# Kernel tuning notes

Hardware: AMD Instinct MI355X
Metric: run time of the kernel (lower is better)

## Reference

```python
import jax, jax.numpy as jnp
import numpy as np

N_HEADS = 4
N_NODES = 10000
EMB = 128
N_BATCH = 4096
N_NEAREST = 8
N_SENTINELS = 8


def setup_inputs() -> dict:
    key = jax.random.key(0)
    k1, k2, k3, k4 = jax.random.split(key, 4)
    embeds = jax.random.normal(k1, (N_HEADS, N_NODES, EMB), jnp.float32)
    field = jax.random.uniform(k3, (N_HEADS, N_NODES, EMB), dtype=jnp.float32)
    uncertainty = jnp.ones((1, 1, 1), jnp.float32) * 5.0
    adj = (jax.random.uniform(k4, (N_NODES, N_NODES)) < 0.001).astype(jnp.float32)
    batch_edges = jax.random.randint(k2, (2, N_BATCH), 0, N_NODES)
    return {"embeds": embeds, "field": field, "uncertainty": uncertainty,
            "adj": adj, "batch_edges": batch_edges}


def _knn_samples(embeds, nodes, k):
    # embeds: (h, n, d); nodes: (b,) -> indices of k nearest neighbors, excluding self.
    # Squared L2 distance is monotone in L2 norm, so top-k order matches the
    # original's .norm(dim=3).topk(..., largest=False).
    x = embeds[:, nodes]                                  # (h, b, d)
    x2 = jnp.sum(x * x, axis=-1)[:, :, None]              # (h, b, 1)
    y2 = jnp.sum(embeds * embeds, axis=-1)[:, None, :]    # (h, 1, n)
    d2 = x2 + y2 - 2.0 * jnp.einsum('hbd,hnd->hbn', x, embeds)  # (h, b, n)
    _, idx = jax.lax.top_k(-d2, k + 1)                    # nearest first
    return jax.lax.stop_gradient(idx[:, :, 1:])           # drop self -> (h, b, k)


def reference(embeds, field, uncertainty, adj, batch_edges):
    src, dst = batch_edges[0], batch_edges[1]
    h_idx = jnp.arange(N_HEADS)[:, None, None]

    def build(nodes, nodes_logits, adj_gather):
        samples = _knn_samples(embeds, nodes, N_NEAREST)                 # (h,b,k)
        diff = embeds[:, nodes][:, :, None, :] - embeds[h_idx, samples]  # (h,b,k,d)
        label = uncertainty * (adj_gather(samples) * 2.0 - 1.0)          # (h,b,k)
        g = field[:, nodes_logits]                                        # (h,b,d)
        logits = jnp.einsum('hbkd,hbd->hbk', diff, g) + label
        return logits, diff

    src_logits, src_diff = build(src, dst, lambda s: adj[s, dst[None, :, None]])
    tgt_logits, tgt_diff = build(dst, src, lambda s: adj[src[None, :, None], s])

    logits = jnp.concatenate([src_logits, tgt_logits], axis=2)           # (h,b,2k)
    dist = jnp.linalg.norm(jnp.concatenate([src_diff, tgt_diff], axis=2), axis=3)

    h, b = logits.shape[0], logits.shape[1]
    logits = jnp.concatenate(
        [logits, jnp.zeros((h, b, N_SENTINELS), logits.dtype)], axis=2)
    dist = jnp.concatenate(
        [dist, jnp.ones((h, b, N_SENTINELS), dist.dtype)], axis=2)

    # softmin: softmax(1 - dist)-weighted sum of logits, then mean over heads
    softmin = jnp.sum(logits * jax.nn.softmax(1.0 - dist, axis=2), axis=2)  # (h,b)
    return jax.nn.sigmoid(softmin.mean(axis=0)).reshape(-1)                 # (b,)
```

## Files before the change

kernel.cpp:

```cpp
#include <hip/hip_runtime.h>
#include <math.h>
#include <stdint.h>

#define N_HEADS 4
#define N_NODES 10000
#define NPAD 10112
#define NPG (NPAD / 32)
#define EMB 128
#define N_BATCH 4096
#define NQ (2 * N_BATCH)
#define K 8
#define TQ 64
#define TN 128
#define NTILES (NPAD / TN)
#define PH 2
#define CAP 41
#define WIN 0.5f

typedef __attribute__((ext_vector_type(8))) __bf16 bf16x8;
typedef __attribute__((ext_vector_type(8))) unsigned short ushortx8;
typedef __attribute__((ext_vector_type(16))) float floatx16;

__device__ __forceinline__ unsigned short f2bf(float x) {
  unsigned u = __float_as_uint(x);
  u += 0x7fff + ((u >> 16) & 1);
  return (unsigned short)(u >> 16);
}
__device__ __forceinline__ uint32_t bfup(float f) {
  uint32_t u = __float_as_uint(f);
  return (f >= 0.f) ? ((u + 0xFFFFu) >> 16) : (u >> 16);
}

__device__ __forceinline__ void insert8(float* bs, int* bi, float s, int node) {
  if (s < bs[K - 1]) {
    #pragma unroll
    for (int k2 = K - 1; k2 >= 0; --k2) {
      if (!(s < bs[k2])) break;
      if (k2 < K - 1) { bs[k2 + 1] = bs[k2]; bi[k2 + 1] = bi[k2]; }
      bs[k2] = s; bi[k2] = node;
    }
  }
}

__device__ __forceinline__ size_t pchunk(int g, int c, int lm) {
  return (size_t)g * 4096 + (size_t)(c >> 1) * 512 + (size_t)(c & 1) * 256 + lm * 8;
}

__global__ __launch_bounds__(256) void prep_kernel(
    const float* __restrict__ E, unsigned short* __restrict__ EhiP,
    float* __restrict__ y2g) {
  __shared__ float s_p[8][33];
  const int h = blockIdx.y, g = blockIdx.x;
  const int lm = threadIdx.x & 31, c8 = threadIdx.x >> 5;
  const int n = g * 32 + lm;
  float x[16];
  #pragma unroll
  for (int j = 0; j < 16; ++j) x[j] = 0.f;
  if (n < N_NODES) {
    const float* src = E + (size_t)(h * N_NODES + n) * EMB + c8 * 16;
    #pragma unroll
    for (int j = 0; j < 4; ++j) {
      float4 v = *(const float4*)(src + j * 4);
      x[j * 4 + 0] = v.x; x[j * 4 + 1] = v.y; x[j * 4 + 2] = v.z; x[j * 4 + 3] = v.w;
    }
  }
  float part = 0.f;
  ushortx8 hi[2];
  #pragma unroll
  for (int j = 0; j < 16; ++j) {
    part += x[j] * x[j];
    hi[j >> 3][j & 7] = f2bf(x[j]);
  }
  size_t base = (size_t)h * NPG * 4096;
  #pragma unroll
  for (int lh = 0; lh < 2; ++lh)
    *(ushortx8*)&EhiP[base + pchunk(g, c8 * 2 + lh, lm)] = hi[lh];
  s_p[c8][lm] = part;
  __syncthreads();
  if (threadIdx.x < 32) {
    int nn = g * 32 + threadIdx.x;
    float s = 0.f;
    #pragma unroll
    for (int j = 0; j < 8; ++j) s += s_p[j][threadIdx.x];
    y2g[h * NPAD + nn] = (nn < N_NODES) ? s : 1e30f;
  }
}

__global__ __launch_bounds__(256)
__attribute__((amdgpu_waves_per_eu(2, 2)))
void knn_kernel(
    const unsigned short* __restrict__ EhiP, const float* __restrict__ y2g,
    const float* __restrict__ Ef, const int* __restrict__ be,
    int* __restrict__ samples) {
  __shared__ __align__(16) float s_x[TQ * TN];
  __shared__ float s_t8S[TQ * 9];
  __shared__ int   s_t8I[TQ * 9];
  __shared__ float s_lsS[TQ * CAP];
  __shared__ int   s_lsI[TQ * CAP];
  __shared__ float s_thr[TQ];
  __shared__ int   s_cnt[TQ];

  const int id = blockIdx.x;
  const int h = (id & 7) >> 1;
  const int qt = ((id >> 3) << 1) | (id & 1);
  const int tid = threadIdx.x;
  const int lane = tid & 63;
  const int w1 = tid >> 6;
  const int lm = lane & 31, lh = lane >> 5;
  const unsigned short* EhiH = EhiP + (size_t)h * NPG * 4096;
  const float* y2H = y2g + h * NPAD;
  const float* EH = Ef + (size_t)h * N_NODES * EMB;

  bf16x8 a0[8], a1[8];
  {
    int q0 = be[qt * TQ + lm];
    int q1 = be[qt * TQ + 32 + lm];
    int g0 = q0 >> 5, l0 = q0 & 31;
    int g1 = q1 >> 5, l1 = q1 & 31;
    #pragma unroll
    for (int ks = 0; ks < 8; ++ks) {
      a0[ks] = *(const bf16x8*)&EhiH[pchunk(g0, ks * 2 + lh, l0)];
      a1[ks] = *(const bf16x8*)&EhiH[pchunk(g1, ks * 2 + lh, l1)];
    }
  }

  const int qsel = tid >> 2;
  const int csel = tid & 3;
  const int myq = be[qt * TQ + qsel];
  float bs[K]; int bi[K];
  #pragma unroll
  for (int k2 = 0; k2 < K; ++k2) { bs[k2] = 1e30f; bi[k2] = 0x7fffffff; }
  if (tid < TQ) s_cnt[tid] = 0;

  const int bnode = 32 * w1 + lm;
  const unsigned short* bhp = EhiH + (size_t)w1 * 4096 + lane * 8;

  #pragma unroll 1
  for (int t = 0; t < PH; ++t) {
    const size_t goff = (size_t)t * 16384;
    float ny = y2H[t * TN + bnode];
    floatx16 acc0 = {0.f, 0.f, 0.f, 0.f, 0.f, 0.f, 0.f, 0.f,
                     0.f, 0.f, 0.f, 0.f, 0.f, 0.f, 0.f, 0.f};
    floatx16 acc1 = acc0;
    #pragma unroll
    for (int ks = 0; ks < 8; ++ks) {
      bf16x8 vbh = *(const bf16x8*)(bhp + goff + ks * 512);
      acc0 = __builtin_amdgcn_mfma_f32_32x32x16_bf16(a0[ks], vbh, acc0, 0, 0, 0);
      acc1 = __builtin_amdgcn_mfma_f32_32x32x16_bf16(a1[ks], vbh, acc1, 0, 0, 0);
    }
    #pragma unroll
    for (int r = 0; r < 16; ++r) {
      int row = (r & 3) + 8 * (r >> 2) + 4 * lh;
      s_x[row * TN + bnode] = fmaf(-2.f, acc0[r], ny);
      s_x[(row + 32) * TN + bnode] = fmaf(-2.f, acc1[r], ny);
    }
    __syncthreads();
    int nbp = t * TN;
    #pragma unroll
    for (int s = 0; s < 32; ++s) {
      int j = csel * 32 + ((s + qsel) & 31);
      float sc = s_x[qsel * TN + j];
      int node = nbp + j;
      if (node != myq) insert8(bs, bi, sc, node);
    }
    __syncthreads();
  }

  {
    float* scrS = (float*)s_x;
    int*   scrI = (int*)s_x + TQ * 32;
    #pragma unroll
    for (int k2 = 0; k2 < K; ++k2) {
      scrS[tid * 8 + k2] = bs[k2]; scrI[tid * 8 + k2] = bi[k2];
    }
    __syncthreads();
    if (tid < TQ) {
      int q = tid;
      float ts[K]; int ti[K];
      #pragma unroll
      for (int k2 = 0; k2 < K; ++k2) { ts[k2] = 1e30f; ti[k2] = 0x7fffffff; }
      for (int kk = 0; kk < 32; ++kk) {
        int e = (kk + q) & 31;
        insert8(ts, ti, scrS[q * 32 + e], scrI[q * 32 + e]);
      }
      float thr = ts[K - 1], win = thr + WIN;
      int nc = 0;
      for (int kk = 0; kk < 32; ++kk) {
        int e = (kk + q) & 31;
        float sv = scrS[q * 32 + e]; int iv = scrI[q * 32 + e];
        if (sv <= win && nc < CAP) {
          bool dup = false;
          #pragma unroll
          for (int j = 0; j < K; ++j) dup = dup || (ti[j] == iv);
          if (!dup) { s_lsS[q * CAP + nc] = sv; s_lsI[q * CAP + nc] = iv; ++nc; }
        }
      }
      s_cnt[q] = nc;
      s_thr[q] = win;
      #pragma unroll
      for (int k2 = 0; k2 < K; ++k2) { s_t8S[q * 9 + k2] = ts[k2]; s_t8I[q * 9 + k2] = ti[k2]; }
    }
    __syncthreads();
  }

  uint32_t thrp0[8], thrp1[8];
  float thmax0, thmax1;
  {
    thmax0 = -1e30f; thmax1 = -1e30f;
    #pragma unroll
    for (int j = 0; j < 8; ++j) {
      int r0 = 2 * j, r1 = 2 * j + 1;
      int w0 = (r0 & 3) + 8 * (r0 >> 2) + 4 * lh;
      int w1r = (r1 & 3) + 8 * (r1 >> 2) + 4 * lh;
      float t00 = s_thr[w0], t01 = s_thr[w1r];
      float t10 = s_thr[w0 + 32], t11 = s_thr[w1r + 32];
      thrp0[j] = bfup(t00) | (bfup(t01) << 16);
      thrp1[j] = bfup(t10) | (bfup(t11) << 16);
      thmax0 = fmaxf(thmax0, fmaxf(t00, t01));
      thmax1 = fmaxf(thmax1, fmaxf(t10, t11));
    }
  }

  #pragma unroll 1
  for (int t = PH; t < NTILES; ++t) {
    if (t == 4 || t == 8 || t == 16 || t == 32) {
      __syncthreads();
      if (tid < TQ) {
        int q = tid;
        int myqm = be[qt * TQ + q];
        float ts[K]; int ti[K];
        #pragma unroll
        for (int k2 = 0; k2 < K; ++k2) { ts[k2] = s_t8S[q * 9 + k2]; ti[k2] = s_t8I[q * 9 + k2]; }
        int cnt = s_cnt[q]; if (cnt > CAP) cnt = CAP;
        for (int p = 0; p < cnt; ++p) {
          int iv = s_lsI[q * CAP + p];
          if (iv != myqm) insert8(ts, ti, s_lsS[q * CAP + p], iv);
        }
        float thr = ts[K - 1], win = thr + WIN;
        int nc = 0;
        for (int p = 0; p < cnt; ++p) {
          float sv = s_lsS[q * CAP + p]; int iv = s_lsI[q * CAP + p];
          if (sv <= win && iv != myqm) {
            bool dup = false;
            #pragma unroll
            for (int j = 0; j < K; ++j) dup = dup || (ti[j] == iv);
            if (!dup && nc < CAP) { s_lsS[q * CAP + nc] = sv; s_lsI[q * CAP + nc] = iv; ++nc; }
          }
        }
        #pragma unroll
        for (int k2 = 0; k2 < K; ++k2) {
          float sv = s_t8S[q * 9 + k2]; int iv = s_t8I[q * 9 + k2];
          if (sv <= win && iv != myqm && nc < CAP) {
            bool dup = false;
            #pragma unroll
            for (int j = 0; j < K; ++j) dup = dup || (ti[j] == iv);
            if (!dup) { s_lsS[q * CAP + nc] = sv; s_lsI[q * CAP + nc] = iv; ++nc; }
          }
        }
        s_cnt[q] = nc;
        s_thr[q] = win;
        #pragma unroll
        for (int k2 = 0; k2 < K; ++k2) { s_t8S[q * 9 + k2] = ts[k2]; s_t8I[q * 9 + k2] = ti[k2]; }
      }
      __syncthreads();
      thmax0 = -1e30f; thmax1 = -1e30f;
      #pragma unroll
      for (int j = 0; j < 8; ++j) {
        int r0 = 2 * j, r1 = 2 * j + 1;
        int w0 = (r0 & 3) + 8 * (r0 >> 2) + 4 * lh;
        int w1r = (r1 & 3) + 8 * (r1 >> 2) + 4 * lh;
        float t00 = s_thr[w0], t01 = s_thr[w1r];
        float t10 = s_thr[w0 + 32], t11 = s_thr[w1r + 32];
        thrp0[j] = bfup(t00) | (bfup(t01) << 16);
        thrp1[j] = bfup(t10) | (bfup(t11) << 16);
        thmax0 = fmaxf(thmax0, fmaxf(t00, t01));
        thmax1 = fmaxf(thmax1, fmaxf(t10, t11));
      }
    }

    const size_t goff = (size_t)t * 16384;
    float ny = y2H[t * TN + bnode];
    floatx16 acc0 = {0.f, 0.f, 0.f, 0.f, 0.f, 0.f, 0.f, 0.f,
                     0.f, 0.f, 0.f, 0.f, 0.f, 0.f, 0.f, 0.f};
    floatx16 acc1 = acc0;
    #pragma unroll
    for (int ks = 0; ks < 8; ++ks) {
      bf16x8 vbh = *(const bf16x8*)(bhp + goff + ks * 512);
      acc0 = __builtin_amdgcn_mfma_f32_32x32x16_bf16(a0[ks], vbh, acc0, 0, 0, 0);
      acc1 = __builtin_amdgcn_mfma_f32_32x32x16_bf16(a1[ks], vbh, acc1, 0, 0, 0);
    }
    const int node = t * TN + bnode;

    {
      float sc[16];
      #pragma unroll
      for (int r = 0; r < 16; ++r) sc[r] = fmaf(-2.f, acc0[r], ny);
      float mn = sc[0];
      #pragma unroll
      for (int r = 1; r < 16; ++r) mn = fminf(mn, sc[r]);
      if (mn < thmax0) {
        #pragma unroll
        for (int r = 0; r < 16; ++r) {
          float th = (r & 1) ? __uint_as_float(thrp0[r >> 1] & 0xFFFF0000u)
                             : __uint_as_float(thrp0[r >> 1] << 16);
          if (sc[r] < th) {
            int q = (r & 3) + 8 * (r >> 2) + 4 * lh;
            int p = atomicAdd(&s_cnt[q], 1);
            if (p < CAP) { s_lsS[q * CAP + p] = sc[r]; s_lsI[q * CAP + p] = node; }
          }
        }
      }
    }
    {
      float sc[16];
      #pragma unroll
      for (int r = 0; r < 16; ++r) sc[r] = fmaf(-2.f, acc1[r], ny);
      float mn = sc[0];
      #pragma unroll
      for (int r = 1; r < 16; ++r) mn = fminf(mn, sc[r]);
      if (mn < thmax1) {
        #pragma unroll
        for (int r = 0; r < 16; ++r) {
          float th = (r & 1) ? __uint_as_float(thrp1[r >> 1] & 0xFFFF0000u)
                             : __uint_as_float(thrp1[r >> 1] << 16);
          if (sc[r] < th) {
            int q = 32 + (r & 3) + 8 * (r >> 2) + 4 * lh;
            int p = atomicAdd(&s_cnt[q], 1);
            if (p < CAP) { s_lsS[q * CAP + p] = sc[r]; s_lsI[q * CAP + p] = node; }
          }
        }
      }
    }
  }

  __syncthreads();
  {
    int q = tid >> 2, k4 = tid & 3;
    int qn = be[qt * TQ + q];
    const float4* Eq = (const float4*)(EH + (size_t)qn * EMB);
    #pragma unroll
    for (int kk = 0; kk < 2; ++kk) {
      int k = k4 + kk * 4;
      int iv = s_t8I[q * 9 + k];
      if (iv < N_NODES) {
        const float4* En = (const float4*)(EH + (size_t)iv * EMB);
        float d0 = 0.f, d1 = 0.f, d2 = 0.f, d3 = 0.f;
        #pragma unroll
        for (int d = 0; d < 32; ++d) {
          float4 a = Eq[d], b = En[d];
          d0 += a.x * b.x; d1 += a.y * b.y; d2 += a.z * b.z; d3 += a.w * b.w;
        }
        s_t8S[q * 9 + k] = y2H[iv] - 2.f * ((d0 + d1) + (d2 + d3));
      }
    }
    int cnt = s_cnt[q]; if (cnt > CAP) cnt = CAP;
    for (int p = k4; p < cnt; p += 4) {
      int jv = s_lsI[q * CAP + p];
      if (jv < N_NODES && jv != qn) {
        const float4* En = (const float4*)(EH + (size_t)jv * EMB);
        float d0 = 0.f, d1 = 0.f, d2 = 0.f, d3 = 0.f;
        #pragma unroll
        for (int d = 0; d < 32; ++d) {
          float4 a = Eq[d], b = En[d];
          d0 += a.x * b.x; d1 += a.y * b.y; d2 += a.z * b.z; d3 += a.w * b.w;
        }
        s_lsS[q * CAP + p] = y2H[jv] - 2.f * ((d0 + d1) + (d2 + d3));
      }
    }
  }
  __syncthreads();
  if (tid < TQ) {
    int q = tid;
    int myqm = be[qt * TQ + q];
    float ts[K]; int ti[K];
    #pragma unroll
    for (int k2 = 0; k2 < K; ++k2) { ts[k2] = 1e30f; ti[k2] = 0x7fffffff; }
    #pragma unroll
    for (int k2 = 0; k2 < K; ++k2)
      insert8(ts, ti, s_t8S[q * 9 + k2], s_t8I[q * 9 + k2]);
    int cnt = s_cnt[q]; if (cnt > CAP) cnt = CAP;
    for (int p = 0; p < cnt; ++p) {
      int iv = s_lsI[q * CAP + p];
      if (iv != myqm) insert8(ts, ti, s_lsS[q * CAP + p], iv);
    }
    size_t base = ((size_t)h * NQ + qt * TQ + q) * K;
    #pragma unroll
    for (int k2 = 0; k2 < K; ++k2) samples[base + k2] = ti[k2];
  }
}

__global__ __launch_bounds__(256) void predict_kernel(
    const float* __restrict__ E, const float* __restrict__ F,
    const float* __restrict__ unc, const float* __restrict__ adj,
    const int* __restrict__ be, const int* __restrict__ samples,
    float* __restrict__ out) {
  int b = blockIdx.x;
  int h = threadIdx.x >> 6;
  int lane = threadIdx.x & 63;
  __shared__ float smv[N_HEADS];

  int srcb = be[b];
  int dstb = be[N_BATCH + b];
  const float* Eh = E + (size_t)h * N_NODES * EMB;
  const float* Fh = F + (size_t)h * N_NODES * EMB;
  float2 es = *(const float2*)(Eh + (size_t)srcb * EMB + 2 * lane);
  float2 ed = *(const float2*)(Eh + (size_t)dstb * EMB + 2 * lane);
  float2 fs = *(const float2*)(Fh + (size_t)srcb * EMB + 2 * lane);
  float2 fd = *(const float2*)(Fh + (size_t)dstb * EMB + 2 * lane);
  float u = unc[0];

  float logit[16], dist[16];
  #pragma unroll
  for (int j = 0; j < 16; ++j) {
    bool isrc = (j < 8);
    int qrow = isrc ? b : (N_BATCH + b);
    int s = samples[((size_t)h * NQ + qrow) * K + (j & 7)];
    float2 ev = *(const float2*)(Eh + (size_t)s * EMB + 2 * lane);
    float2 bb = isrc ? es : ed;
    float2 g = isrc ? fd : fs;
    float dx = bb.x - ev.x, dy = bb.y - ev.y;
    float dot = dx * g.x + dy * g.y;
    float nrm = dx * dx + dy * dy;
    #pragma unroll
    for (int o = 32; o > 0; o >>= 1) {
      dot += __shfl_xor(dot, o);
      nrm += __shfl_xor(nrm, o);
    }
    float a = isrc ? adj[(size_t)s * N_NODES + dstb]
                   : adj[(size_t)srcb * N_NODES + s];
    logit[j] = dot + u * (2.0f * a - 1.0f);
    dist[j] = sqrtf(nrm);
  }

  float m = 0.0f;
  #pragma unroll
  for (int j = 0; j < 16; ++j) m = fmaxf(m, 1.0f - dist[j]);
  float Z = 8.0f * expf(-m);
  float num = 0.0f;
  #pragma unroll
  for (int j = 0; j < 16; ++j) {
    float e = expf(1.0f - dist[j] - m);
    Z += e;
    num += logit[j] * e;
  }
  if (lane == 0) smv[h] = num / Z;
  __syncthreads();
  if (threadIdx.x == 0) {
    float t = 0.25f * (smv[0] + smv[1] + smv[2] + smv[3]);
    out[b] = 1.0f / (1.0f + expf(-t));
  }
}

extern "C" void kernel_launch(void* const* d_in, const int* in_sizes, int n_in,
                              void* d_out, int out_size, void* d_ws,
                              size_t ws_size, hipStream_t stream) {
  const float* E = (const float*)d_in[0];
  const float* F = (const float*)d_in[1];
  const float* U = (const float*)d_in[2];
  const float* A = (const float*)d_in[3];
  const int* be = (const int*)d_in[4];
  float* out = (float*)d_out;

  char* w = (char*)d_ws;
  unsigned short* EhiP = (unsigned short*)(w);
  float* y2g = (float*)(w + 10354688);
  int* samples = (int*)(w + 10516736);

  prep_kernel<<<dim3(NPG, N_HEADS), 256, 0, stream>>>(E, EhiP, y2g);
  knn_kernel<<<dim3((NQ / TQ) * N_HEADS), 256, 0, stream>>>(EhiP, y2g, E, be, samples);
  predict_kernel<<<dim3(N_BATCH), 256, 0, stream>>>(E, F, U, A, be, samples, out);
}
```

Baseline: 809.7 us.

## Widen KNN node tile to 256 with 512-thread blocks and drop min-prefilter

Doubles the node tile per iteration to 256 (padding nodes to 10240) and launches the KNN kernel with 512 threads (8 waves), so each block has twice as many waves covering node columns. The initial exact top-8 seeding now runs on a single wider tile, splitting the two query halves through a smaller shared scratch, and threshold refreshes move to earlier tile indices. The per-fragment min/threshold-max early-out before the candidate-threshold checks is removed to cut per-element work. The aim is more parallelism and fewer loop iterations, at the cost of higher register and occupancy pressure and branchier candidate filtering.

```diff
diff --git a/kernel.cpp b/kernel.cpp
--- a/kernel.cpp
+++ b/kernel.cpp
@@ -4,16 +4,15 @@
 
 #define N_HEADS 4
 #define N_NODES 10000
-#define NPAD 10112
+#define NPAD 10240
 #define NPG (NPAD / 32)
 #define EMB 128
 #define N_BATCH 4096
 #define NQ (2 * N_BATCH)
 #define K 8
 #define TQ 64
-#define TN 128
+#define TN 256
 #define NTILES (NPAD / TN)
-#define PH 2
 #define CAP 41
 #define WIN 0.5f
 
@@ -86,13 +85,13 @@
   }
 }
 
-__global__ __launch_bounds__(256)
-__attribute__((amdgpu_waves_per_eu(2, 2)))
+__global__ __launch_bounds__(512)
+__attribute__((amdgpu_waves_per_eu(4, 4)))
 void knn_kernel(
     const unsigned short* __restrict__ EhiP, const float* __restrict__ y2g,
     const float* __restrict__ Ef, const int* __restrict__ be,
     int* __restrict__ samples) {
-  __shared__ __align__(16) float s_x[TQ * TN];
+  __shared__ __align__(16) float s_x[32 * TN];
   __shared__ float s_t8S[TQ * 9];
   __shared__ int   s_t8I[TQ * 9];
   __shared__ float s_lsS[TQ * CAP];
@@ -124,8 +123,8 @@
     }
   }
 
-  const int qsel = tid >> 2;
-  const int csel = tid & 3;
+  const int qsel = tid >> 3;
+  const int csel = tid & 7;
   const int myq = be[qt * TQ + qsel];
   float bs[K]; int bi[K];
   #pragma unroll
@@ -135,16 +134,14 @@
   const int bnode = 32 * w1 + lm;
   const unsigned short* bhp = EhiH + (size_t)w1 * 4096 + lane * 8;
 
-  #pragma unroll 1
-  for (int t = 0; t < PH; ++t) {
-    const size_t goff = (size_t)t * 16384;
-    float ny = y2H[t * TN + bnode];
+  {
+    float ny = y2H[bnode];
     floatx16 acc0 = {0.f, 0.f, 0.f, 0.f, 0.f, 0.f, 0.f, 0.f,
                      0.f, 0.f, 0.f, 0.f, 0.f, 0.f, 0.f, 0.f};
     floatx16 acc1 = acc0;
     #pragma unroll
     for (int ks = 0; ks < 8; ++ks) {
-      bf16x8 vbh = *(const bf16x8*)(bhp + goff + ks * 512);
+      bf16x8 vbh = *(const bf16x8*)(bhp + ks * 512);
       acc0 = __builtin_amdgcn_mfma_f32_32x32x16_bf16(a0[ks], vbh, acc0, 0, 0, 0);
       acc1 = __builtin_amdgcn_mfma_f32_32x32x16_bf16(a1[ks], vbh, acc1, 0, 0, 0);
     }
@@ -152,23 +149,37 @@
     for (int r = 0; r < 16; ++r) {
       int row = (r & 3) + 8 * (r >> 2) + 4 * lh;
       s_x[row * TN + bnode] = fmaf(-2.f, acc0[r], ny);
-      s_x[(row + 32) * TN + bnode] = fmaf(-2.f, acc1[r], ny);
-    }
-    __syncthreads();
-    int nbp = t * TN;
-    #pragma unroll
-    for (int s = 0; s < 32; ++s) {
-      int j = csel * 32 + ((s + qsel) & 31);
-      float sc = s_x[qsel * TN + j];
-      int node = nbp + j;
-      if (node != myq) insert8(bs, bi, sc, node);
+    }
+    __syncthreads();
+    if (qsel < 32) {
+      #pragma unroll
+      for (int s = 0; s < 32; ++s) {
+        int j = csel * 32 + ((s + qsel) & 31);
+        float sc = s_x[qsel * TN + j];
+        if (j != myq) insert8(bs, bi, sc, j);
+      }
+    }
+    __syncthreads();
+    #pragma unroll
+    for (int r = 0; r < 16; ++r) {
+      int row = (r & 3) + 8 * (r >> 2) + 4 * lh;
+      s_x[row * TN + bnode] = fmaf(-2.f, acc1[r], ny);
+    }
+    __syncthreads();
+    if (qsel >= 32) {
+      #pragma unroll
+      for (int s = 0; s < 32; ++s) {
+        int j = csel * 32 + ((s + qsel) & 31);
+        float sc = s_x[(qsel - 32) * TN + j];
+        if (j != myq) insert8(bs, bi, sc, j);
+      }
     }
     __syncthreads();
   }
 
   {
     float* scrS = (float*)s_x;
-    int*   scrI = (int*)s_x + TQ * 32;
+    int*   scrI = (int*)s_x + 4096;
     #pragma unroll
     for (int k2 = 0; k2 < K; ++k2) {
       scrS[tid * 8 + k2] = bs[k2]; scrI[tid * 8 + k2] = bi[k2];
@@ -179,15 +190,15 @@
       float ts[K]; int ti[K];
       #pragma unroll
       for (int k2 = 0; k2 < K; ++k2) { ts[k2] = 1e30f; ti[k2] = 0x7fffffff; }
-      for (int kk = 0; kk < 32; ++kk) {
-        int e = (kk + q) & 31;
-        insert8(ts, ti, scrS[q * 32 + e], scrI[q * 32 + e]);
+      for (int kk = 0; kk < 64; ++kk) {
+        int e = (kk + q) & 63;
+        insert8(ts, ti, scrS[q * 64 + e], scrI[q * 64 + e]);
       }
       float thr = ts[K - 1], win = thr + WIN;
       int nc = 0;
-      for (int kk = 0; kk < 32; ++kk) {
-        int e = (kk + q) & 31;
-        float sv = scrS[q * 32 + e]; int iv = scrI[q * 32 + e];
+      for (int kk = 0; kk < 64; ++kk) {
+        int e = (kk + q) & 63;
+        float sv = scrS[q * 64 + e]; int iv = scrI[q * 64 + e];
         if (sv <= win && nc < CAP) {
           bool dup = false;
           #pragma unroll
@@ -204,26 +215,18 @@
   }
 
   uint32_t thrp0[8], thrp1[8];
-  float thmax0, thmax1;
-  {
-    thmax0 = -1e30f; thmax1 = -1e30f;
-    #pragma unroll
-    for (int j = 0; j < 8; ++j) {
-      int r0 = 2 * j, r1 = 2 * j + 1;
-      int w0 = (r0 & 3) + 8 * (r0 >> 2) + 4 * lh;
-      int w1r = (r1 & 3) + 8 * (r1 >> 2) + 4 * lh;
-      float t00 = s_thr[w0], t01 = s_thr[w1r];
-      float t10 = s_thr[w0 + 32], t11 = s_thr[w1r + 32];
-      thrp0[j] = bfup(t00) | (bfup(t01) << 16);
-      thrp1[j] = bfup(t10) | (bfup(t11) << 16);
-      thmax0 = fmaxf(thmax0, fmaxf(t00, t01));
-      thmax1 = fmaxf(thmax1, fmaxf(t10, t11));
-    }
+  #pragma unroll
+  for (int j = 0; j < 8; ++j) {
+    int r0 = 2 * j, r1 = 2 * j + 1;
+    int w0 = (r0 & 3) + 8 * (r0 >> 2) + 4 * lh;
+    int w1r = (r1 & 3) + 8 * (r1 >> 2) + 4 * lh;
+    thrp0[j] = bfup(s_thr[w0]) | (bfup(s_thr[w1r]) << 16);
+    thrp1[j] = bfup(s_thr[w0 + 32]) | (bfup(s_thr[w1r + 32]) << 16);
   }
 
   #pragma unroll 1
-  for (int t = PH; t < NTILES; ++t) {
-    if (t == 4 || t == 8 || t == 16 || t == 32) {
+  for (int t = 1; t < NTILES; ++t) {
+    if (t == 2 || t == 4 || t == 8 || t == 16) {
       __syncthreads();
       if (tid < TQ) {
         int q = tid;
@@ -263,22 +266,17 @@
         for (int k2 = 0; k2 < K; ++k2) { s_t8S[q * 9 + k2] = ts[k2]; s_t8I[q * 9 + k2] = ti[k2]; }
       }
       __syncthreads();
-      thmax0 = -1e30f; thmax1 = -1e30f;
       #pragma unroll
       for (int j = 0; j < 8; ++j) {
         int r0 = 2 * j, r1 = 2 * j + 1;
         int w0 = (r0 & 3) + 8 * (r0 >> 2) + 4 * lh;
         int w1r = (r1 & 3) + 8 * (r1 >> 2) + 4 * lh;
-        float t00 = s_thr[w0], t01 = s_thr[w1r];
-        float t10 = s_thr[w0 + 32], t11 = s_thr[w1r + 32];
-        thrp0[j] = bfup(t00) | (bfup(t01) << 16);
-        thrp1[j] = bfup(t10) | (bfup(t11) << 16);
-        thmax0 = fmaxf(thmax0, fmaxf(t00, t01));
-        thmax1 = fmaxf(thmax1, fmaxf(t10, t11));
-      }
-    }
-
-    const size_t goff = (size_t)t * 16384;
+        thrp0[j] = bfup(s_thr[w0]) | (bfup(s_thr[w1r]) << 16);
+        thrp1[j] = bfup(s_thr[w0 + 32]) | (bfup(s_thr[w1r + 32]) << 16);
+      }
+    }
+
+    const size_t goff = (size_t)t * 32768;
     float ny = y2H[t * TN + bnode];
     floatx16 acc0 = {0.f, 0.f, 0.f, 0.f, 0.f, 0.f, 0.f, 0.f,
                      0.f, 0.f, 0.f, 0.f, 0.f, 0.f, 0.f, 0.f};
@@ -290,71 +288,48 @@
       acc1 = __builtin_amdgcn_mfma_f32_32x32x16_bf16(a1[ks], vbh, acc1, 0, 0, 0);
     }
     const int node = t * TN + bnode;
-
-    {
-      float sc[16];
-      #pragma unroll
-      for (int r = 0; r < 16; ++r) sc[r] = fmaf(-2.f, acc0[r], ny);
-      float mn = sc[0];
-      #pragma unroll
-      for (int r = 1; r < 16; ++r) mn = fminf(mn, sc[r]);
-      if (mn < thmax0) {
-        #pragma unroll
-        for (int r = 0; r < 16; ++r) {
-          float th = (r & 1) ? __uint_as_float(thrp0[r >> 1] & 0xFFFF0000u)
-                             : __uint_as_float(thrp0[r >> 1] << 16);
-          if (sc[r] < th) {
-            int q = (r & 3) + 8 * (r >> 2) + 4 * lh;
-            int p = atomicAdd(&s_cnt[q], 1);
-            if (p < CAP) { s_lsS[q * CAP + p] = sc[r]; s_lsI[q * CAP + p] = node; }
-          }
-        }
-      }
-    }
-    {
-      float sc[16];
-      #pragma unroll
-      for (int r = 0; r < 16; ++r) sc[r] = fmaf(-2.f, acc1[r], ny);
-      float mn = sc[0];
-      #pragma unroll
-      for (int r = 1; r < 16; ++r) mn = fminf(mn, sc[r]);
-      if (mn < thmax1) {
-        #pragma unroll
-        for (int r = 0; r < 16; ++r) {
-          float th = (r & 1) ? __uint_as_float(thrp1[r >> 1] & 0xFFFF0000u)
-                             : __uint_as_float(thrp1[r >> 1] << 16);
-          if (sc[r] < th) {
-            int q = 32 + (r & 3) + 8 * (r >> 2) + 4 * lh;
-            int p = atomicAdd(&s_cnt[q], 1);
-            if (p < CAP) { s_lsS[q * CAP + p] = sc[r]; s_lsI[q * CAP + p] = node; }
-          }
-        }
+    #pragma unroll
+    for (int r = 0; r < 16; ++r) {
+      float sc = fmaf(-2.f, acc0[r], ny);
+      float th = (r & 1) ? __uint_as_float(thrp0[r >> 1] & 0xFFFF0000u)
+                         : __uint_as_float(thrp0[r >> 1] << 16);
+      if (sc < th) {
+        int q = (r & 3) + 8 * (r >> 2) + 4 * lh;
+        int p = atomicAdd(&s_cnt[q], 1);
+        if (p < CAP) { s_lsS[q * CAP + p] = sc; s_lsI[q * CAP + p] = node; }
+      }
+    }
+    #pragma unroll
+    for (int r = 0; r < 16; ++r) {
+      float sc = fmaf(-2.f, acc1[r], ny);
+      float th = (r & 1) ? __uint_as_float(thrp1[r >> 1] & 0xFFFF0000u)
+                         : __uint_as_float(thrp1[r >> 1] << 16);
+      if (sc < th) {
+        int q = 32 + (r & 3) + 8 * (r >> 2) + 4 * lh;
+        int p = atomicAdd(&s_cnt[q], 1);
+        if (p < CAP) { s_lsS[q * CAP + p] = sc; s_lsI[q * CAP + p] = node; }
       }
     }
   }
 
   __syncthreads();
   {
-    int q = tid >> 2, k4 = tid & 3;
+    int q = tid >> 3, k = tid & 7;
     int qn = be[qt * TQ + q];
     const float4* Eq = (const float4*)(EH + (size_t)qn * EMB);
-    #pragma unroll
-    for (int kk = 0; kk < 2; ++kk) {
-      int k = k4 + kk * 4;
-      int iv = s_t8I[q * 9 + k];
-      if (iv < N_NODES) {
-        const float4* En = (const float4*)(EH + (size_t)iv * EMB);
-        float d0 = 0.f, d1 = 0.f, d2 = 0.f, d3 = 0.f;
-        #pragma unroll
-        for (int d = 0; d < 32; ++d) {
-          float4 a = Eq[d], b = En[d];
-          d0 += a.x * b.x; d1 += a.y * b.y; d2 += a.z * b.z; d3 += a.w * b.w;
-        }
-        s_t8S[q * 9 + k] = y2H[iv] - 2.f * ((d0 + d1) + (d2 + d3));
-      }
+    int iv = s_t8I[q * 9 + k];
+    if (iv < N_NODES) {
+      const float4* En = (const float4*)(EH + (size_t)iv * EMB);
+      float d0 = 0.f, d1 = 0.f, d2 = 0.f, d3 = 0.f;
+      #pragma unroll
+      for (int d = 0; d < 32; ++d) {
+        float4 a = Eq[d], b = En[d];
+        d0 += a.x * b.x; d1 += a.y * b.y; d2 += a.z * b.z; d3 += a.w * b.w;
+      }
+      s_t8S[q * 9 + k] = y2H[iv] - 2.f * ((d0 + d1) + (d2 + d3));
     }
     int cnt = s_cnt[q]; if (cnt > CAP) cnt = CAP;
-    for (int p = k4; p < cnt; p += 4) {
+    for (int p = k; p < cnt; p += 8) {
       int jv = s_lsI[q * CAP + p];
       if (jv < N_NODES && jv != qn) {
         const float4* En = (const float4*)(EH + (size_t)jv * EMB);
@@ -463,10 +438,10 @@
 
   char* w = (char*)d_ws;
   unsigned short* EhiP = (unsigned short*)(w);
-  float* y2g = (float*)(w + 10354688);
-  int* samples = (int*)(w + 10516736);
+  float* y2g = (float*)(w + 10485760);
+  int* samples = (int*)(w + 10649600);
 
   prep_kernel<<<dim3(NPG, N_HEADS), 256, 0, stream>>>(E, EhiP, y2g);
-  knn_kernel<<<dim3((NQ / TQ) * N_HEADS), 256, 0, stream>>>(EhiP, y2g, E, be, samples);
+  knn_kernel<<<dim3((NQ / TQ) * N_HEADS), 512, 0, stream>>>(EhiP, y2g, E, be, samples);
   predict_kernel<<<dim3(N_BATCH), 256, 0, stream>>>(E, F, U, A, be, samples, out);
 }
```

Measured after the change: 962.0 us. +18.8%, slower.

## Double-buffer B-tile register prefetch and drop per-tile min early-exit check

Applied to the files above, without the earlier changes.

The tile loop now advances two tiles per iteration. It loads the next tile's bf16 B fragments and y2 norms into a second register buffer while the current tile's MFMAs and threshold filtering run, so global-load latency overlaps compute. The thmax early-exit (min over 16 scores compared to the max threshold) is removed, and every score is compared against its per-row threshold directly. The extra buffer adds about 64 VGPRs, which may reduce occupancy. The threshold refresh points still fall on even tile indices, so they stay aligned with the new stride.

```diff
diff --git a/kernel.cpp b/kernel.cpp
--- a/kernel.cpp
+++ b/kernel.cpp
@@ -204,25 +204,65 @@
   }
 
   uint32_t thrp0[8], thrp1[8];
-  float thmax0, thmax1;
-  {
-    thmax0 = -1e30f; thmax1 = -1e30f;
-    #pragma unroll
-    for (int j = 0; j < 8; ++j) {
-      int r0 = 2 * j, r1 = 2 * j + 1;
-      int w0 = (r0 & 3) + 8 * (r0 >> 2) + 4 * lh;
-      int w1r = (r1 & 3) + 8 * (r1 >> 2) + 4 * lh;
-      float t00 = s_thr[w0], t01 = s_thr[w1r];
-      float t10 = s_thr[w0 + 32], t11 = s_thr[w1r + 32];
-      thrp0[j] = bfup(t00) | (bfup(t01) << 16);
-      thrp1[j] = bfup(t10) | (bfup(t11) << 16);
-      thmax0 = fmaxf(thmax0, fmaxf(t00, t01));
-      thmax1 = fmaxf(thmax1, fmaxf(t10, t11));
-    }
-  }
+  #pragma unroll
+  for (int j = 0; j < 8; ++j) {
+    int r0 = 2 * j, r1 = 2 * j + 1;
+    int w0 = (r0 & 3) + 8 * (r0 >> 2) + 4 * lh;
+    int w1r = (r1 & 3) + 8 * (r1 >> 2) + 4 * lh;
+    thrp0[j] = bfup(s_thr[w0]) | (bfup(s_thr[w1r]) << 16);
+    thrp1[j] = bfup(s_thr[w0 + 32]) | (bfup(s_thr[w1r + 32]) << 16);
+  }
+
+#define PREFETCH_T(VB, NY, TT)                                               \
+  do {                                                                       \
+    const size_t goff_ = (size_t)(TT) * 16384;                               \
+    NY = y2H[(TT) * TN + bnode];                                             \
+    _Pragma("unroll")                                                        \
+    for (int ks = 0; ks < 8; ++ks)                                           \
+      VB[ks] = *(const bf16x8*)(bhp + goff_ + ks * 512);                     \
+  } while (0)
+
+#define COMPUTE_T(VB, NY, TT)                                                \
+  do {                                                                       \
+    floatx16 acc0 = {0.f, 0.f, 0.f, 0.f, 0.f, 0.f, 0.f, 0.f,                 \
+                     0.f, 0.f, 0.f, 0.f, 0.f, 0.f, 0.f, 0.f};                \
+    floatx16 acc1 = acc0;                                                    \
+    _Pragma("unroll")                                                        \
+    for (int ks = 0; ks < 8; ++ks) {                                         \
+      acc0 = __builtin_amdgcn_mfma_f32_32x32x16_bf16(a0[ks], VB[ks], acc0, 0, 0, 0); \
+      acc1 = __builtin_amdgcn_mfma_f32_32x32x16_bf16(a1[ks], VB[ks], acc1, 0, 0, 0); \
+    }                                                                        \
+    const int node_ = (TT) * TN + bnode;                                     \
+    _Pragma("unroll")                                                        \
+    for (int r = 0; r < 16; ++r) {                                           \
+      float sc = fmaf(-2.f, acc0[r], NY);                                    \
+      float th = (r & 1) ? __uint_as_float(thrp0[r >> 1] & 0xFFFF0000u)      \
+                         : __uint_as_float(thrp0[r >> 1] << 16);             \
+      if (sc < th) {                                                         \
+        int q_ = (r & 3) + 8 * (r >> 2) + 4 * lh;                            \
+        int p_ = atomicAdd(&s_cnt[q_], 1);                                   \
+        if (p_ < CAP) { s_lsS[q_ * CAP + p_] = sc; s_lsI[q_ * CAP + p_] = node_; } \
+      }                                                                      \
+    }                                                                        \
+    _Pragma("unroll")                                                        \
+    for (int r = 0; r < 16; ++r) {                                           \
+      float sc = fmaf(-2.f, acc1[r], NY);                                    \
+      float th = (r & 1) ? __uint_as_float(thrp1[r >> 1] & 0xFFFF0000u)      \
+                         : __uint_as_float(thrp1[r >> 1] << 16);             \
+      if (sc < th) {                                                         \
+        int q_ = 32 + (r & 3) + 8 * (r >> 2) + 4 * lh;                       \
+        int p_ = atomicAdd(&s_cnt[q_], 1);                                   \
+        if (p_ < CAP) { s_lsS[q_ * CAP + p_] = sc; s_lsI[q_ * CAP + p_] = node_; } \
+      }                                                                      \
+    }                                                                        \
+  } while (0)
+
+  bf16x8 vbA[8], vbB[8];
+  float nyA = 0.f, nyB = 0.f;
+  PREFETCH_T(vbA, nyA, PH);
 
   #pragma unroll 1
-  for (int t = PH; t < NTILES; ++t) {
+  for (int t = PH; t < NTILES; t += 2) {
     if (t == 4 || t == 8 || t == 16 || t == 32) {
       __syncthreads();
       if (tid < TQ) {
@@ -263,75 +303,25 @@
         for (int k2 = 0; k2 < K; ++k2) { s_t8S[q * 9 + k2] = ts[k2]; s_t8I[q * 9 + k2] = ti[k2]; }
       }
       __syncthreads();
-      thmax0 = -1e30f; thmax1 = -1e30f;
       #pragma unroll
       for (int j = 0; j < 8; ++j) {
         int r0 = 2 * j, r1 = 2 * j + 1;
         int w0 = (r0 & 3) + 8 * (r0 >> 2) + 4 * lh;
         int w1r = (r1 & 3) + 8 * (r1 >> 2) + 4 * lh;
-        float t00 = s_thr[w0], t01 = s_thr[w1r];
-        float t10 = s_thr[w0 + 32], t11 = s_thr[w1r + 32];
-        thrp0[j] = bfup(t00) | (bfup(t01) << 16);
-        thrp1[j] = bfup(t10) | (bfup(t11) << 16);
-        thmax0 = fmaxf(thmax0, fmaxf(t00, t01));
-        thmax1 = fmaxf(thmax1, fmaxf(t10, t11));
-      }
-    }
-
-    const size_t goff = (size_t)t * 16384;
-    float ny = y2H[t * TN + bnode];
-    floatx16 acc0 = {0.f, 0.f, 0.f, 0.f, 0.f, 0.f, 0.f, 0.f,
-                     0.f, 0.f, 0.f, 0.f, 0.f, 0.f, 0.f, 0.f};
-    floatx16 acc1 = acc0;
-    #pragma unroll
-    for (int ks = 0; ks < 8; ++ks) {
-      bf16x8 vbh = *(const bf16x8*)(bhp + goff + ks * 512);
-      acc0 = __builtin_amdgcn_mfma_f32_32x32x16_bf16(a0[ks], vbh, acc0, 0, 0, 0);
-      acc1 = __builtin_amdgcn_mfma_f32_32x32x16_bf16(a1[ks], vbh, acc1, 0, 0, 0);
-    }
-    const int node = t * TN + bnode;
-
-    {
-      float sc[16];
-      #pragma unroll
-      for (int r = 0; r < 16; ++r) sc[r] = fmaf(-2.f, acc0[r], ny);
-      float mn = sc[0];
-      #pragma unroll
-      for (int r = 1; r < 16; ++r) mn = fminf(mn, sc[r]);
-      if (mn < thmax0) {
-        #pragma unroll
-        for (int r = 0; r < 16; ++r) {
-          float th = (r & 1) ? __uint_as_float(thrp0[r >> 1] & 0xFFFF0000u)
-                             : __uint_as_float(thrp0[r >> 1] << 16);
-          if (sc[r] < th) {
-            int q = (r & 3) + 8 * (r >> 2) + 4 * lh;
-            int p = atomicAdd(&s_cnt[q], 1);
-            if (p < CAP) { s_lsS[q * CAP + p] = sc[r]; s_lsI[q * CAP + p] = node; }
-          }
-        }
-      }
-    }
-    {
-      float sc[16];
-      #pragma unroll
-      for (int r = 0; r < 16; ++r) sc[r] = fmaf(-2.f, acc1[r], ny);
-      float mn = sc[0];
-      #pragma unroll
-      for (int r = 1; r < 16; ++r) mn = fminf(mn, sc[r]);
-      if (mn < thmax1) {
-        #pragma unroll
-        for (int r = 0; r < 16; ++r) {
-          float th = (r & 1) ? __uint_as_float(thrp1[r >> 1] & 0xFFFF0000u)
-                             : __uint_as_float(thrp1[r >> 1] << 16);
-          if (sc[r] < th) {
-            int q = 32 + (r & 3) + 8 * (r >> 2) + 4 * lh;
-            int p = atomicAdd(&s_cnt[q], 1);
-            if (p < CAP) { s_lsS[q * CAP + p] = sc[r]; s_lsI[q * CAP + p] = node; }
-          }
-        }
-      }
-    }
-  }
+        thrp0[j] = bfup(s_thr[w0]) | (bfup(s_thr[w1r]) << 16);
+        thrp1[j] = bfup(s_thr[w0 + 32]) | (bfup(s_thr[w1r + 32]) << 16);
+      }
+    }
+
+    if (t + 1 < NTILES) PREFETCH_T(vbB, nyB, t + 1);
+    COMPUTE_T(vbA, nyA, t);
+    if (t + 1 < NTILES) {
+      if (t + 2 < NTILES) PREFETCH_T(vbA, nyA, t + 2);
+      COMPUTE_T(vbB, nyB, t + 1);
+    }
+  }
+#undef PREFETCH_T
+#undef COMPUTE_T
 
   __syncthreads();
   {
```

New measurement: 781.8 us. -3.4%, faster.
